# Kernel tuning notes

Hardware: AMD Instinct MI355X
Metric: run time of the kernel (lower is better)

## Reference

```python
import jax, jax.numpy as jnp
import numpy as np
import math

D_MODEL = 2048
N_HEADS = 32
N_KV_HEADS = 8
HEAD_DIM = D_MODEL // N_HEADS  # 64
N_GROUPS = N_HEADS // N_KV_HEADS  # 4
MAX_SEQ_LEN = 2048
ROPE_THETA = 500000.0


def precompute_rope(head_dim, max_seq_len, theta=ROPE_THETA):
    freqs = 1.0 / theta ** (jnp.arange(0, head_dim, 2, dtype=jnp.float32) / head_dim)
    positions = jnp.arange(max_seq_len, dtype=jnp.float32)
    angles = jnp.outer(positions, freqs)  # [S, head_dim/2]
    return jnp.cos(angles), jnp.sin(angles)


def apply_rope(x, cos, sin):
    # x: [B, H, S, D]; cos/sin: [S, D/2]
    half = x.shape[-1] // 2
    x1, x2 = x[..., :half], x[..., half:]
    cos = cos[None, None]
    sin = sin[None, None]
    return jnp.concatenate([x1 * cos - x2 * sin, x1 * sin + x2 * cos], axis=-1)


def setup_inputs() -> dict:
    key = jax.random.key(0)
    k1, k2, k3, k4, k5 = jax.random.split(key, 5)
    B, S = 2, 2048
    x = jax.random.normal(k1, (B, S, D_MODEL), dtype=jnp.float32)
    sd = 1.0 / math.sqrt(D_MODEL)
    # weights stored as [in, out] so forward is x @ W (same math as torch Linear)
    W_q = jax.random.normal(k2, (D_MODEL, N_HEADS * HEAD_DIM), dtype=jnp.float32) * sd
    W_k = jax.random.normal(k3, (D_MODEL, N_KV_HEADS * HEAD_DIM), dtype=jnp.float32) * sd
    W_v = jax.random.normal(k4, (D_MODEL, N_KV_HEADS * HEAD_DIM), dtype=jnp.float32) * sd
    W_o = jax.random.normal(k5, (N_HEADS * HEAD_DIM, D_MODEL), dtype=jnp.float32) * sd
    cos, sin = precompute_rope(HEAD_DIM, MAX_SEQ_LEN)
    return {"x": x, "W_q": W_q, "W_k": W_k, "W_v": W_v, "W_o": W_o,
            "rope_cos": cos, "rope_sin": sin}


def reference(x, W_q, W_k, W_v, W_o, rope_cos, rope_sin):
    B, S, _ = x.shape
    scale = 1.0 / math.sqrt(HEAD_DIM)
    # projections -> [B, H, S, D]
    q = (x @ W_q).reshape(B, S, N_HEADS, HEAD_DIM).transpose(0, 2, 1, 3)
    k = (x @ W_k).reshape(B, S, N_KV_HEADS, HEAD_DIM).transpose(0, 2, 1, 3)
    v = (x @ W_v).reshape(B, S, N_KV_HEADS, HEAD_DIM).transpose(0, 2, 1, 3)
    # RoPE
    q = apply_rope(q, rope_cos[:S], rope_sin[:S])
    k = apply_rope(k, rope_cos[:S], rope_sin[:S])
    # GQA expand: repeat each KV head n_groups times
    k = jnp.repeat(k, N_GROUPS, axis=1)  # [B, H, S, D]
    v = jnp.repeat(v, N_GROUPS, axis=1)
    # scores + causal mask + softmax
    scores = jnp.einsum('bhqd,bhkd->bhqk', q, k) * scale
    causal = jnp.tril(jnp.ones((S, S), dtype=bool))
    scores = jnp.where(causal[None, None], scores, -jnp.inf)
    weights = jax.nn.softmax(scores, axis=-1)
    attn_out = jnp.einsum('bhqk,bhkd->bhqd', weights, v)
    out = attn_out.transpose(0, 2, 1, 3).reshape(B, S, N_HEADS * HEAD_DIM) @ W_o
    return out
```

## Files before the change

### kernel.cpp

```cpp
#include <hip/hip_runtime.h>
#include <hip/hip_bf16.h>

typedef __attribute__((ext_vector_type(8))) short short8;
typedef __attribute__((ext_vector_type(4))) short short4v;
typedef __attribute__((ext_vector_type(4))) float f32x4;

#define MFMA(A,B,C) __builtin_amdgcn_mfma_f32_16x16x32_bf16(A,B,C,0,0,0)
#define SW(row) ((((row) & 3)) | (((row) >> 1) & 4))
#define SCL 0.18033688f

__device__ __forceinline__ short f2bs(float f) {
    __hip_bfloat16 h = __float2bfloat16(f);
    union { __hip_bfloat16 h; short s; } u; u.h = h; return u.s;
}

__device__ __forceinline__ float exp2v(float x) {
    float r; asm("v_exp_f32 %0, %1" : "=v"(r) : "v"(x)); return r;
}

__device__ __forceinline__ unsigned cvtpk(float a, float b) {
    unsigned r; asm("v_cvt_pk_bf16_f32 %0, %1, %2" : "=v"(r) : "v"(a), "v"(b)); return r;
}

__device__ __forceinline__ void async16(void* lds, const void* g) {
    __builtin_amdgcn_global_load_lds(
        (const __attribute__((address_space(1))) unsigned int*)g,
        (__attribute__((address_space(3))) unsigned int*)lds, 16, 0, 0);
}

__global__ __launch_bounds__(256) void prep_k(
    const float* __restrict__ x,
    const float* __restrict__ Wq, const float* __restrict__ Wk,
    const float* __restrict__ Wv, const float* __restrict__ Wo,
    short* __restrict__ x_bf, short* __restrict__ Wqkv_t, short* __restrict__ Wo_t)
{
    __shared__ float tile[32][33];
    int bid = blockIdx.x;
    const int t = threadIdx.x;

    if (bid < 8192) {
        int i = bid * 256 + t;
        const float4 v = *(const float4*)(x + (size_t)i * 4);
        short4v o;
        o.x = f2bs(v.x); o.y = f2bs(v.y); o.z = f2bs(v.z); o.w = f2bs(v.w);
        *(short4v*)(x_bf + (size_t)i * 4) = o;
        return;
    }
    bid -= 8192;

    const float* W; short* Wt; int nbx;
    const int K = 2048;
    if (bid < 4096)      { W = Wq; Wt = Wqkv_t;                          nbx = 64; }
    else if (bid < 5120) { bid -= 4096; W = Wk; Wt = Wqkv_t + (size_t)2048 * 2048; nbx = 16; }
    else if (bid < 6144) { bid -= 5120; W = Wv; Wt = Wqkv_t + (size_t)2560 * 2048; nbx = 16; }
    else                 { bid -= 6144; W = Wo; Wt = Wo_t;               nbx = 64; }
    const int N = nbx * 32;
    const int tx = t & 31, ty = t >> 5;
    const int n0 = (bid % nbx) * 32, k0 = (bid / nbx) * 32;

    #pragma unroll
    for (int i = 0; i < 32; i += 8)
        tile[ty + i][tx] = W[(size_t)(k0 + ty + i) * N + n0 + tx];
    __syncthreads();
    #pragma unroll
    for (int i = 0; i < 32; i += 8)
        Wt[(size_t)(n0 + ty + i) * K + k0 + tx] = f2bs(tile[tx][ty + i]);
}

__global__ __launch_bounds__(512, 2) void gemm_qkv_k(
    const short* __restrict__ A, const short* __restrict__ Bt,
    short* __restrict__ Cq, short* __restrict__ Ck, short* __restrict__ Cv,
    const float* __restrict__ rc, const float* __restrict__ rs,
    int M, int N, int K)
{
    extern __shared__ short lds[];
    const int t = threadIdx.x;
    const int l = t & 63, w = t >> 6;
    const int lo = l & 15, hi = l >> 4;
    const int wm = w >> 2, wn = w & 3;
    const int lr = l >> 3, ls = l & 7;

    const int nbx = gridDim.x;
    const int nwg = nbx * gridDim.y;
    const int bid0 = blockIdx.y * nbx + blockIdx.x;
    const int wg = (bid0 & 7) * (nwg >> 3) + (bid0 >> 3);
    const int tm = (wg % nbx) * 256, tn = (wg / nbx) * 256;

    const f32x4 z4 = {0.f, 0.f, 0.f, 0.f};
    f32x4 acc[8][4];
    #pragma unroll
    for (int m = 0; m < 8; ++m)
        #pragma unroll
        for (int n = 0; n < 4; ++n) acc[m][n] = z4;

    auto stage_half = [&](int kt, int buf, int h) {
        const size_t ko = (size_t)kt * 64;
        const short* src = (h < 2) ? A : Bt;
        const int rbase = (h == 1 || h == 3) ? 128 : 0;
        const int gbase = (h < 2) ? tm : tn;
        short* dst = lds + buf * 32768 + ((h < 2) ? 0 : 16384) + rbase * 64;
        #pragma unroll
        for (int j = 0; j < 2; ++j) {
            int g = w * 2 + j;
            int row = g * 8 + lr;
            int gs = ls ^ SW(row);
            async16(dst + g * 512, src + (size_t)(gbase + rbase + row) * K + ko + gs * 8);
        }
    };

    const int nkt = K >> 6;
    #pragma unroll
    for (int h = 0; h < 4; ++h) stage_half(0, 0, h);
    __syncthreads();

    int cur = 0;
    for (int kt = 0; kt < nkt; ++kt) {
        const bool pf = (kt + 1 < nkt);
        const short* Ab_ = lds + cur * 32768;
        const short* Bb_ = Ab_ + 16384;
        short8 af[4], bfr[4];
        #pragma unroll
        for (int ph = 0; ph < 4; ++ph) {
            const int ks = ph >> 1, mh = ph & 1;
            const int slot = ks * 4 + hi;
            #pragma unroll
            for (int mm = 0; mm < 4; ++mm) {
                int row = wm * 128 + (mh * 4 + mm) * 16 + lo;
                af[mm] = *(const short8*)(Ab_ + row * 64 + ((slot ^ SW(row)) << 3));
            }
            if (mh == 0) {
                #pragma unroll
                for (int n = 0; n < 4; ++n) {
                    int row = wn * 64 + n * 16 + lo;
                    bfr[n] = *(const short8*)(Bb_ + row * 64 + ((slot ^ SW(row)) << 3));
                }
            }
            if (pf && ph < 2) {
                stage_half(kt + 1, cur ^ 1, ph * 2);
                stage_half(kt + 1, cur ^ 1, ph * 2 + 1);
            }
            __builtin_amdgcn_s_barrier();
            asm volatile("s_waitcnt lgkmcnt(0)" ::: "memory");
            __builtin_amdgcn_sched_barrier(0);
            __builtin_amdgcn_s_setprio(1);
            #pragma unroll
            for (int n = 0; n < 4; ++n)
                #pragma unroll
                for (int mm = 0; mm < 4; ++mm)
                    acc[mh * 4 + mm][n] = MFMA(af[mm], bfr[n], acc[mh * 4 + mm][n]);
            __builtin_amdgcn_s_setprio(0);
            if (ph == 3 && pf)
                asm volatile("s_waitcnt vmcnt(0)" ::: "memory");
            __builtin_amdgcn_s_barrier();
        }
        cur ^= 1;
    }

    const int ctn = tn + wn * 64;
    if (ctn < 2048) {
        #pragma unroll
        for (int m = 0; m < 8; ++m)
            #pragma unroll
            for (int r = 0; r < 4; ++r) {
                int row = tm + wm * 128 + m * 16 + hi * 4 + r;
                int b = row >> 11, s = row & 2047;
                #pragma unroll
                for (int n = 0; n < 2; ++n) {
                    int col = ctn + n * 16 + lo;
                    int h = col >> 6, d = col & 63;
                    float x1 = acc[m][n][r], x2 = acc[m][n + 2][r];
                    float c = rc[s * 32 + d], sn = rs[s * 32 + d];
                    size_t base = (((size_t)b * 32 + h) * 2048 + s) * 64;
                    Cq[base + d]      = f2bs((x1 * c - x2 * sn) * SCL);
                    Cq[base + d + 32] = f2bs((x1 * sn + x2 * c) * SCL);
                }
            }
    } else if (ctn < 2560) {
        #pragma unroll
        for (int m = 0; m < 8; ++m)
            #pragma unroll
            for (int r = 0; r < 4; ++r) {
                int row = tm + wm * 128 + m * 16 + hi * 4 + r;
                int b = row >> 11, s = row & 2047;
                #pragma unroll
                for (int n = 0; n < 2; ++n) {
                    int col = ctn - 2048 + n * 16 + lo;
                    int h = col >> 6, d = col & 63;
                    float x1 = acc[m][n][r], x2 = acc[m][n + 2][r];
                    float c = rc[s * 32 + d], sn = rs[s * 32 + d];
                    size_t base = (((size_t)b * 8 + h) * 2048 + s) * 64;
                    Ck[base + d]      = f2bs(x1 * c - x2 * sn);
                    Ck[base + d + 32] = f2bs(x1 * sn + x2 * c);
                }
            }
    } else {
        #pragma unroll
        for (int m = 0; m < 8; ++m)
            #pragma unroll
            for (int r = 0; r < 4; ++r) {
                int row = tm + wm * 128 + m * 16 + hi * 4 + r;
                int b = row >> 11, s = row & 2047;
                #pragma unroll
                for (int n = 0; n < 4; ++n) {
                    int col = ctn - 2560 + n * 16 + lo;
                    int h = col >> 6, d = col & 63;
                    Cv[(((size_t)b * 8 + h) * 64 + d) * 2048 + s] = f2bs(acc[m][n][r]);
                }
            }
    }
}

__global__ __launch_bounds__(512, 2) void gemm_o_k(
    const short* __restrict__ A, const short* __restrict__ Bt,
    float* __restrict__ Cf, int M, int N, int K)
{
    extern __shared__ short lds[];
    const int t = threadIdx.x;
    const int l = t & 63, w = t >> 6;
    const int lo = l & 15, hi = l >> 4;
    const int wm = w >> 2, wn = w & 3;
    const int lr = l >> 3, ls = l & 7;

    const int nbx = gridDim.x;
    const int nwg = nbx * gridDim.y;
    const int bid0 = blockIdx.y * nbx + blockIdx.x;
    const int wg = (bid0 & 7) * (nwg >> 3) + (bid0 >> 3);
    const int tm = (wg % nbx) * 128, tn = (wg / nbx) * 256;

    const f32x4 z4 = {0.f, 0.f, 0.f, 0.f};
    f32x4 acc[4][4];
    #pragma unroll
    for (int m = 0; m < 4; ++m)
        #pragma unroll
        for (int n = 0; n < 4; ++n) acc[m][n] = z4;

    const int srow = w * 8 + lr;
    const int sswz = ls ^ SW(srow);

    auto stage_unit = [&](int kt, int buf, int u) {
        const size_t ko = (size_t)kt * 64;
        short* base = lds + buf * 24576;
        if (u < 2)
            async16(base + u * 4096 + w * 512,
                    A + (size_t)(tm + u * 64 + srow) * K + ko + sswz * 8);
        else
            async16(base + 8192 + (u - 2) * 4096 + w * 512,
                    Bt + (size_t)(tn + (u - 2) * 64 + srow) * K + ko + sswz * 8);
    };

    const int nkt = K >> 6;
    #pragma unroll
    for (int u = 0; u < 6; ++u) stage_unit(0, 0, u);
    #pragma unroll
    for (int u = 0; u < 6; ++u) stage_unit(1, 1, u);
    asm volatile("s_waitcnt vmcnt(6)" ::: "memory");
    __builtin_amdgcn_s_barrier();

    int cur = 0;
    for (int kt = 0; kt < nkt; ++kt) {
        int tgt = cur + 2; if (tgt >= 3) tgt -= 3;
        const bool pf2 = (kt + 2 < nkt);
        const bool pf1 = (kt + 1 < nkt);
        const short* Ab_ = lds + cur * 24576;
        const short* Bb_ = Ab_ + 8192;
        short8 af[4], bfr[4];
        #pragma unroll
        for (int ph = 0; ph < 2; ++ph) {
            const int slot = ph * 4 + hi;
            #pragma unroll
            for (int mm = 0; mm < 4; ++mm) {
                int row = wm * 64 + mm * 16 + lo;
                af[mm] = *(const short8*)(Ab_ + row * 64 + ((slot ^ SW(row)) << 3));
            }
            #pragma unroll
            for (int n = 0; n < 4; ++n) {
                int row = wn * 64 + n * 16 + lo;
                bfr[n] = *(const short8*)(Bb_ + row * 64 + ((slot ^ SW(row)) << 3));
            }
            if (pf2) {
                stage_unit(kt + 2, tgt, ph * 3);
                stage_unit(kt + 2, tgt, ph * 3 + 1);
                stage_unit(kt + 2, tgt, ph * 3 + 2);
            }
            __builtin_amdgcn_s_barrier();
            asm volatile("s_waitcnt lgkmcnt(0)" ::: "memory");
            __builtin_amdgcn_sched_barrier(0);
            __builtin_amdgcn_s_setprio(1);
            #pragma unroll
            for (int n = 0; n < 4; ++n)
                #pragma unroll
                for (int mm = 0; mm < 4; ++mm)
                    acc[mm][n] = MFMA(af[mm], bfr[n], acc[mm][n]);
            __builtin_amdgcn_s_setprio(0);
            if (ph == 1) {
                if (pf2)      asm volatile("s_waitcnt vmcnt(6)" ::: "memory");
                else if (pf1) asm volatile("s_waitcnt vmcnt(0)" ::: "memory");
            }
            __builtin_amdgcn_s_barrier();
        }
        cur = (cur == 2) ? 0 : cur + 1;
    }

    #pragma unroll
    for (int m = 0; m < 4; ++m)
        #pragma unroll
        for (int r = 0; r < 4; ++r) {
            int row = tm + wm * 64 + m * 16 + hi * 4 + r;
            #pragma unroll
            for (int n = 0; n < 4; ++n) {
                int col = tn + wn * 64 + n * 16 + lo;
                Cf[(size_t)row * N + col] = acc[m][n][r];
            }
        }
}

__global__ __launch_bounds__(256) void attn_k(
    const short* __restrict__ Qp, const short* __restrict__ Kp, const short* __restrict__ Vt,
    short* __restrict__ Ab)
{
    __shared__ short KV[2][8192];
    const int t = threadIdx.x, l = t & 63, w = t >> 6;
    const int lo = l & 15, hi = l >> 4;
    const int lr = l >> 3, ls = l & 7;
    const int pair = blockIdx.x;
    const int h = blockIdx.y, b = blockIdx.z;
    const int kvh = h >> 2;
    const size_t qbase  = (size_t)(b * 32 + h) * 2048 * 64;
    const size_t kbase  = (size_t)(b * 8 + kvh) * 2048 * 64;
    const size_t vtbase = (size_t)(b * 8 + kvh) * 64 * 2048;
    const size_t abase  = (size_t)b * 2048 * 2048 + (size_t)h * 64;

    for (int halfq = 0; halfq < 2; ++halfq) {
        const int qtile = halfq ? 31 - pair : pair;
        const int nkt = qtile + 1;

        short8 qf[2];
        {
            int qrow = qtile * 64 + w * 16 + lo;
            #pragma unroll
            for (int ks = 0; ks < 2; ++ks)
                qf[ks] = *(const short8*)(Qp + qbase + (size_t)qrow * 64 + (ks * 4 + hi) * 8);
        }

        const f32x4 z4 = {0.f, 0.f, 0.f, 0.f};
        float l_run = 0.f;
        f32x4 oacc[4];
        #pragma unroll
        for (int nd = 0; nd < 4; ++nd) oacc[nd] = z4;

        #pragma unroll
        for (int j = 0; j < 2; ++j) {
            int g8 = w * 2 + j;
            int row = g8 * 8 + lr;
            int gs = ls ^ SW(row);
            async16(&KV[0][g8 * 512],        Kp + kbase + (size_t)row * 64 + gs * 8);
            async16(&KV[0][4096 + g8 * 512], Vt + vtbase + (size_t)row * 2048 + gs * 8);
        }
        __syncthreads();

        int cur = 0;
        for (int kt = 0; kt < nkt; ++kt) {
            if (kt + 1 < nkt) {
                #pragma unroll
                for (int j = 0; j < 2; ++j) {
                    int g8 = w * 2 + j;
                    int row = g8 * 8 + lr;
                    int gs = ls ^ SW(row);
                    async16(&KV[cur ^ 1][g8 * 512],
                            Kp + kbase + (size_t)((kt + 1) * 64 + row) * 64 + gs * 8);
                    async16(&KV[cur ^ 1][4096 + g8 * 512],
                            Vt + vtbase + (size_t)row * 2048 + (kt + 1) * 64 + gs * 8);
                }
            }

            const short* Ks = &KV[cur][0];
            const short* Vs = &KV[cur][4096];

            f32x4 sacc[4];
            #pragma unroll
            for (int n = 0; n < 4; ++n) sacc[n] = z4;
            __builtin_amdgcn_s_setprio(1);
            #pragma unroll
            for (int ks = 0; ks < 2; ++ks) {
                const int slot = ks * 4 + hi;
                #pragma unroll
                for (int n = 0; n < 4; ++n) {
                    const int krow = ((lo >> 2) << 3) + ((n & 1) << 2) + (lo & 3) + ((n >> 1) << 5);
                    short8 kf = *(const short8*)(Ks + krow * 64 + ((slot ^ SW(krow)) << 3));
                    sacc[n] = MFMA(kf, qf[ks], sacc[n]);
                }
            }
            __builtin_amdgcn_s_setprio(0);

            float p[4][4];
            if (kt == qtile) {
                const int q = qtile * 64 + w * 16 + lo;
                #pragma unroll
                for (int n = 0; n < 4; ++n)
                    #pragma unroll
                    for (int r = 0; r < 4; ++r) {
                        int k = kt * 64 + hi * 8 + ((n & 1) << 2) + r + ((n >> 1) << 5);
                        p[n][r] = exp2v((k > q) ? -3e38f : sacc[n][r]);
                    }
            } else {
                #pragma unroll
                for (int n = 0; n < 4; ++n)
                    #pragma unroll
                    for (int r = 0; r < 4; ++r)
                        p[n][r] = exp2v(sacc[n][r]);
            }
            float rs0 = 0.f, rs1 = 0.f;
            #pragma unroll
            for (int n = 0; n < 4; ++n) {
                rs0 += p[n][0] + p[n][1];
                rs1 += p[n][2] + p[n][3];
            }
            l_run += rs0 + rs1;

            short8 afr[2];
            #pragma unroll
            for (int ks = 0; ks < 2; ++ks) {
                union { short8 s; unsigned u[4]; } pk;
                pk.u[0] = cvtpk(p[2 * ks][0],     p[2 * ks][1]);
                pk.u[1] = cvtpk(p[2 * ks][2],     p[2 * ks][3]);
                pk.u[2] = cvtpk(p[2 * ks + 1][0], p[2 * ks + 1][1]);
                pk.u[3] = cvtpk(p[2 * ks + 1][2], p[2 * ks + 1][3]);
                afr[ks] = pk.s;
            }

            __builtin_amdgcn_s_setprio(1);
            #pragma unroll
            for (int ks = 0; ks < 2; ++ks) {
                const int slot = ks * 4 + hi;
                #pragma unroll
                for (int nd = 0; nd < 4; ++nd) {
                    const int vrow = nd * 16 + lo;
                    short8 vf = *(const short8*)(Vs + vrow * 64 + ((slot ^ SW(vrow)) << 3));
                    oacc[nd] = MFMA(afr[ks], vf, oacc[nd]);
                }
            }
            __builtin_amdgcn_s_setprio(0);

            __syncthreads();
            cur ^= 1;
        }

        l_run += __shfl_xor(l_run, 16, 64);
        l_run += __shfl_xor(l_run, 32, 64);
        float rl[4];
        #pragma unroll
        for (int r = 0; r < 4; ++r)
            rl[r] = 1.0f / __shfl(l_run, (l & 48) | (hi * 4 + r), 64);
        #pragma unroll
        for (int nd = 0; nd < 4; ++nd)
            #pragma unroll
            for (int r = 0; r < 4; ++r) {
                int s = qtile * 64 + w * 16 + hi * 4 + r;
                Ab[abase + (size_t)s * 2048 + nd * 16 + lo] = f2bs(oacc[nd][r] * rl[r]);
            }
    }
}

extern "C" void kernel_launch(void* const* d_in, const int* in_sizes, int n_in,
                              void* d_out, int out_size, void* d_ws, size_t ws_size,
                              hipStream_t stream)
{
    const float* x  = (const float*)d_in[0];
    const float* Wq = (const float*)d_in[1];
    const float* Wk = (const float*)d_in[2];
    const float* Wv = (const float*)d_in[3];
    const float* Wo = (const float*)d_in[4];
    const float* rc = (const float*)d_in[5];
    const float* rs = (const float*)d_in[6];
    float* out = (float*)d_out;
    char* ws = (char*)d_ws;

    size_t off = 0;
    short* x_bf   = (short*)(ws + off); off += (size_t)4096 * 2048 * 2;
    short* Wqkv_t = (short*)(ws + off); off += (size_t)3072 * 2048 * 2;
    short* Wo_t   = (short*)(ws + off); off += (size_t)2048 * 2048 * 2;
    short* Qp     = (short*)(ws + off); off += (size_t)2 * 32 * 2048 * 64 * 2;
    short* Kp     = (short*)(ws + off); off += (size_t)2 * 8 * 2048 * 64 * 2;
    short* Vtb    = (short*)(ws + off); off += (size_t)2 * 8 * 64 * 2048 * 2;
    short* Ab     = (short*)(ws + off); off += (size_t)4096 * 2048 * 2;
    if (off > ws_size) return;

    const int LDS_QKV = 2 * 32768 * 2;
    const int LDS_O   = 3 * 24576 * 2;
    (void)hipFuncSetAttribute((const void*)gemm_qkv_k,
                              hipFuncAttributeMaxDynamicSharedMemorySize, LDS_QKV);
    (void)hipFuncSetAttribute((const void*)gemm_o_k,
                              hipFuncAttributeMaxDynamicSharedMemorySize, LDS_O);

    prep_k<<<18432, 256, 0, stream>>>(x, Wq, Wk, Wv, Wo, x_bf, Wqkv_t, Wo_t);

    gemm_qkv_k<<<dim3(16, 12), 512, LDS_QKV, stream>>>(x_bf, Wqkv_t, Qp, Kp, Vtb,
                                                       rc, rs, 4096, 3072, 2048);

    attn_k<<<dim3(16, 32, 2), 256, 0, stream>>>(Qp, Kp, Vtb, Ab);

    gemm_o_k<<<dim3(32, 8), 512, LDS_O, stream>>>(Ab, Wo_t, out, 4096, 2048, 2048);
}
```

Before: 169.5 us.

## Restructure QKV GEMM pipeline to one barrier per k-tile with per-wave waits

Issues the whole next-tile prefetch at the top of each k-iteration and drops the four barriers per k-tile (with their full lgkmcnt waits) in favour of one barrier at the end. Each wave waits only on the vmcnt count for its own loads that the next tile's reads depend on. B staging is split into row-chunk pieces so the wait counts line up per wave. This is meant to cut synchronisation overhead and let MFMA run without barriers in between. The hand-tuned per-wave vmcnt values are fragile, and relying on them for correctness risks LDS race conditions.

```diff
diff --git a/kernel.cpp b/kernel.cpp
--- a/kernel.cpp
+++ b/kernel.cpp
@@ -78,7 +78,7 @@
     const int l = t & 63, w = t >> 6;
     const int lo = l & 15, hi = l >> 4;
     const int wm = w >> 2, wn = w & 3;
-    const int lr = l >> 3, ls = l & 7;
+    const int lr8 = l >> 3, ls8 = l & 7;
 
     const int nbx = gridDim.x;
     const int nwg = nbx * gridDim.y;
@@ -93,64 +93,87 @@
         #pragma unroll
         for (int n = 0; n < 4; ++n) acc[m][n] = z4;
 
-    auto stage_half = [&](int kt, int buf, int h) {
+    auto stageA = [&](int kt, int buf, int h) {
         const size_t ko = (size_t)kt * 64;
-        const short* src = (h < 2) ? A : Bt;
-        const int rbase = (h == 1 || h == 3) ? 128 : 0;
-        const int gbase = (h < 2) ? tm : tn;
-        short* dst = lds + buf * 32768 + ((h < 2) ? 0 : 16384) + rbase * 64;
+        const int rbase = h * 128;
+        short* dst = lds + buf * 32768 + rbase * 64;
         #pragma unroll
         for (int j = 0; j < 2; ++j) {
             int g = w * 2 + j;
-            int row = g * 8 + lr;
-            int gs = ls ^ SW(row);
-            async16(dst + g * 512, src + (size_t)(gbase + rbase + row) * K + ko + gs * 8);
+            int row = g * 8 + lr8;
+            int gs = ls8 ^ SW(row);
+            async16(dst + g * 512, A + (size_t)(tm + rbase + row) * K + ko + gs * 8);
         }
     };
+    auto stageB = [&](int kt, int buf, int j) {
+        const size_t ko = (size_t)kt * 64;
+        short* dst = lds + buf * 32768 + 16384 + j * 4096 + w * 512;
+        int row = j * 64 + w * 8 + lr8;
+        int gs = ls8 ^ SW(row);
+        async16(dst, Bt + (size_t)(tn + row) * K + ko + gs * 8);
+    };
+    auto stage_tile = [&](int kt, int buf) {
+        stageA(kt, buf, 0);
+        stageB(kt, buf, 0);
+        stageA(kt, buf, 1);
+        stageB(kt, buf, 1);
+        stageB(kt, buf, 2);
+        stageB(kt, buf, 3);
+    };
+    auto wave_wait = [&]() {
+        switch (w) {
+            case 0: asm volatile("s_waitcnt vmcnt(5)" ::: "memory"); break;
+            case 1: asm volatile("s_waitcnt vmcnt(2)" ::: "memory"); break;
+            case 2: asm volatile("s_waitcnt vmcnt(1)" ::: "memory"); break;
+            case 3: asm volatile("s_waitcnt vmcnt(0)" ::: "memory"); break;
+            case 4: asm volatile("s_waitcnt vmcnt(3)" ::: "memory"); break;
+            case 5: asm volatile("s_waitcnt vmcnt(2)" ::: "memory"); break;
+            case 6: asm volatile("s_waitcnt vmcnt(1)" ::: "memory"); break;
+            default: asm volatile("s_waitcnt vmcnt(0)" ::: "memory"); break;
+        }
+    };
 
     const int nkt = K >> 6;
-    #pragma unroll
-    for (int h = 0; h < 4; ++h) stage_half(0, 0, h);
-    __syncthreads();
+    stage_tile(0, 0);
+    wave_wait();
+    __builtin_amdgcn_s_barrier();
 
     int cur = 0;
     for (int kt = 0; kt < nkt; ++kt) {
         const bool pf = (kt + 1 < nkt);
+        if (pf) stage_tile(kt + 1, cur ^ 1);
         const short* Ab_ = lds + cur * 32768;
         const short* Bb_ = Ab_ + 16384;
-        short8 af[4], bfr[4];
-        #pragma unroll
-        for (int ph = 0; ph < 4; ++ph) {
-            const int ks = ph >> 1, mh = ph & 1;
+
+        __builtin_amdgcn_s_setprio(1);
+        #pragma unroll
+        for (int ks = 0; ks < 2; ++ks) {
             const int slot = ks * 4 + hi;
-            #pragma unroll
-            for (int mm = 0; mm < 4; ++mm) {
-                int row = wm * 128 + (mh * 4 + mm) * 16 + lo;
-                af[mm] = *(const short8*)(Ab_ + row * 64 + ((slot ^ SW(row)) << 3));
-            }
-            if (mh == 0) {
-                #pragma unroll
-                for (int n = 0; n < 4; ++n) {
-                    int row = wn * 64 + n * 16 + lo;
-                    bfr[n] = *(const short8*)(Bb_ + row * 64 + ((slot ^ SW(row)) << 3));
-                }
-            }
-            if (pf && ph < 2) {
-                stage_half(kt + 1, cur ^ 1, ph * 2);
-                stage_half(kt + 1, cur ^ 1, ph * 2 + 1);
-            }
-            __builtin_amdgcn_s_barrier();
-            asm volatile("s_waitcnt lgkmcnt(0)" ::: "memory");
-            __builtin_amdgcn_sched_barrier(0);
-            __builtin_amdgcn_s_setprio(1);
-            #pragma unroll
-            for (int n = 0; n < 4; ++n)
-                #pragma unroll
-                for (int mm = 0; mm < 4; ++mm)
-                    acc[mh * 4 + mm][n] = MFMA(af[mm], bfr[n], acc[mh * 4 + mm][n]);
-            __builtin_amdgcn_s_setprio(0);
-            if (ph == 3 && pf)
-                asm volatile("s_waitcnt vmcnt(0)" ::: "memory");
+            short8 bfr[4];
+            #pragma unroll
+            for (int n = 0; n < 4; ++n) {
+                int row = wn * 64 + n * 16 + lo;
+                bfr[n] = *(const short8*)(Bb_ + row * 64 + ((slot ^ SW(row)) << 3));
+            }
+            #pragma unroll
+            for (int mh = 0; mh < 2; ++mh) {
+                short8 af[4];
+                #pragma unroll
+                for (int mm = 0; mm < 4; ++mm) {
+                    int row = wm * 128 + (mh * 4 + mm) * 16 + lo;
+                    af[mm] = *(const short8*)(Ab_ + row * 64 + ((slot ^ SW(row)) << 3));
+                }
+                #pragma unroll
+                for (int n = 0; n < 4; ++n)
+                    #pragma unroll
+                    for (int mm = 0; mm < 4; ++mm)
+                        acc[mh * 4 + mm][n] = MFMA(af[mm], bfr[n], acc[mh * 4 + mm][n]);
+            }
+        }
+        __builtin_amdgcn_s_setprio(0);
+
+        if (pf) {
+            wave_wait();
             __builtin_amdgcn_s_barrier();
         }
         cur ^= 1;
```

Result: no change. 169.4 us, median of 2 (-0.0%).
